# Kernel optimization log

Measured on AMD Instinct MI355X. Metric: run time of the kernel, lower is better.

## Reference

```python
import jax, jax.numpy as jnp
import numpy as np

N_NODES = 100000
N_EDGES = 1600000
DIM = 128
N_LAYERS = 3
BN_EPS = 1e-5


def setup_inputs() -> dict:
    key = jax.random.key(0)
    ks = jax.random.split(key, 8)
    x = jax.random.normal(ks[0], (N_NODES, DIM), dtype=jnp.float32)
    edge_index = jax.random.randint(ks[1], (2, N_EDGES), 0, N_NODES, dtype=jnp.int64)
    batch = jax.random.randint(ks[2], (N_NODES,), 0, 64, dtype=jnp.int64)
    # stacked per-layer params (input_dim == hidden_dim == 128)
    W = jax.random.normal(ks[3], (N_LAYERS, DIM, DIM), dtype=jnp.float32) / np.sqrt(DIM)
    b = jnp.zeros((N_LAYERS, DIM), dtype=jnp.float32)
    gamma = jax.random.normal(ks[4], (N_LAYERS, DIM), dtype=jnp.float32) * 0.1 + 1.0
    beta = jax.random.normal(ks[5], (N_LAYERS, DIM), dtype=jnp.float32) * 0.1
    running_mean = jax.random.normal(ks[6], (N_LAYERS, DIM), dtype=jnp.float32) * 0.1
    running_var = jax.random.uniform(ks[7], (N_LAYERS, DIM), dtype=jnp.float32, minval=0.5, maxval=1.5)
    return {"x": x, "edge_index": edge_index, "batch": batch, "W": W, "b": b,
            "gamma": gamma, "beta": beta,
            "running_mean": running_mean, "running_var": running_var}


def reference(x, edge_index, batch, W, b, gamma, beta, running_mean, running_var):
    # batch is unused by the original forward (kept for signature fidelity)
    n = x.shape[0]
    # GCNConv adds self-loops once per layer; precompute augmented edge list + norm
    loops = jnp.arange(n, dtype=edge_index.dtype)
    src = jnp.concatenate([edge_index[0], loops])
    dst = jnp.concatenate([edge_index[1], loops])
    deg = jax.ops.segment_sum(jnp.ones_like(dst, dtype=x.dtype), dst, num_segments=n)
    dinv = jax.lax.rsqrt(jnp.maximum(deg, 1e-12))
    norm = dinv[src] * dinv[dst]  # [E+N]

    h = x
    for l in range(N_LAYERS):
        # GCNConv: propagate normalized messages of (h @ W), then add bias
        hw = h @ W[l]                                   # [N, D]
        msg = hw[src] * norm[:, None]                   # gather  [E+N, D]
        h = jax.ops.segment_sum(msg, dst, num_segments=n) + b[l]
        # BatchNorm1d (eval mode: running stats) + ReLU; dropout is identity in eval
        h = gamma[l] * (h - running_mean[l]) * jax.lax.rsqrt(running_var[l] + BN_EPS) + beta[l]
        h = jax.nn.relu(h)
    return h
```

## Files before the change

kernel.cpp:

```cpp
#include <hip/hip_runtime.h>

#define N_NODES 100000
#define N_EDGES 1600000
#define DIM 128
#define BN_EPS 1e-5f
#define BM 64
#define BSHIFT 9
#define BN 512
#define NB 196
#define CAP_S 9216
#define CAP_C 10048
#define CHUNK 4096

typedef _Float16 f16;
typedef _Float16 f16x4 __attribute__((ext_vector_type(4)));
typedef _Float16 f16x8 __attribute__((ext_vector_type(8)));
typedef float f32x4 __attribute__((ext_vector_type(4)));


__global__ void k_bzero(int* __restrict__ bcnt) {
  int t = threadIdx.x;
  if (t < NB) bcnt[t] = 0;
}

__global__ __launch_bounds__(256) void k_binA(const int* __restrict__ src,
                                              const int* __restrict__ dst,
                                              int* __restrict__ bcnt,
                                              int2* __restrict__ stage) {
  __shared__ int hist[NB];
  __shared__ int lofs[NB];
  __shared__ int lbase[NB];
  __shared__ int lcur[NB];
  __shared__ int scanbuf[256];
  __shared__ int2 buf[CHUNK];
  int t = threadIdx.x;
  for (int i = t; i < NB; i += 256) { hist[i] = 0; lcur[i] = 0; }
  __syncthreads();
  int e0 = blockIdx.x * CHUNK;
  int en = min(CHUNK, N_EDGES - e0);
  for (int i = t; i < en; i += 256) {
    unsigned d = (unsigned)dst[e0 + i];
    unsigned s = (unsigned)src[e0 + i];
    if (d < N_NODES && s < N_NODES) atomicAdd(&hist[d >> BSHIFT], 1);
  }
  __syncthreads();
  scanbuf[t] = (t < NB) ? hist[t] : 0;
  __syncthreads();
  for (int off = 1; off < 256; off <<= 1) {
    int x = (t >= off) ? scanbuf[t - off] : 0;
    __syncthreads();
    scanbuf[t] += x;
    __syncthreads();
  }
  if (t < NB) {
    lofs[t] = scanbuf[t] - hist[t];
    lbase[t] = atomicAdd(&bcnt[t], hist[t]);
  }
  __syncthreads();
  for (int i = t; i < en; i += 256) {
    int d = dst[e0 + i], s = src[e0 + i];
    if ((unsigned)d < N_NODES && (unsigned)s < N_NODES) {
      int b = d >> BSHIFT;
      int r = atomicAdd(&lcur[b], 1);
      buf[lofs[b] + r] = make_int2(d, s);
    }
  }
  __syncthreads();
  int tot = lofs[NB - 1] + hist[NB - 1];
  for (int i = t; i < tot; i += 256) {
    int2 p = buf[i];
    int b = p.x >> BSHIFT;
    int goff = lbase[b] + (i - lofs[b]);
    if (goff < CAP_S) stage[(size_t)b * CAP_S + goff] = p;
  }
}

__global__ __launch_bounds__(512) void k_binB(const int2* __restrict__ stage,
                                              const int* __restrict__ bcnt,
                                              int* __restrict__ rowpack,
                                              int* __restrict__ col) {
  __shared__ int cnt[BN];
  __shared__ int offs[BN];
  __shared__ int lcur[BN];
  __shared__ int sb[BN];
  __shared__ int mp_s;
  __shared__ int colbuf[CAP_C];
  int b = blockIdx.x, t = threadIdx.x;
  int base = b << BSHIFT;
  int nn = min(BN, N_NODES - base);
  int m = min(bcnt[b], CAP_S);
  const int2* seg = stage + (size_t)b * CAP_S;
  cnt[t] = 0; lcur[t] = 0;
  __syncthreads();
  for (int i = t; i < m; i += 512) atomicAdd(&cnt[seg[i].x - base], 1);
  __syncthreads();
  int pcnt = (cnt[t] + 3) & ~3;
  sb[t] = pcnt;
  __syncthreads();
  for (int off = 1; off < 512; off <<= 1) {
    int x = (t >= off) ? sb[t - off] : 0;
    __syncthreads();
    sb[t] += x;
    __syncthreads();
  }
  offs[t] = sb[t] - pcnt;
  if (t == 511) mp_s = sb[511];
  __syncthreads();
  for (int i = t; i < m; i += 512) {
    int2 p = seg[i];
    int dl = p.x - base;
    int r = atomicAdd(&lcur[dl], 1);
    int o = offs[dl] + r;
    if (o < CAP_C) colbuf[o] = p.y;
  }
  __syncthreads();
  {
    int o = offs[t], c = cnt[t], pc = (c + 3) & ~3;
    for (int k = c; k < pc; k++)
      if (o + k < CAP_C) colbuf[o + k] = N_NODES;
  }
  __syncthreads();
  if (t < nn) {
    int o = offs[t], c = cnt[t];
    if (o + ((c + 3) & ~3) > CAP_C) { o = 0; c = 0; }
    rowpack[base + t] = (o << 14) | c;
  }
  int mp = min(mp_s, CAP_C);
  for (int i = t; i < mp; i += 512) col[b * CAP_C + i] = colbuf[i];
}


__global__ void k_x16(const float* __restrict__ x, f16* __restrict__ h16) {
  int i = blockIdx.x * blockDim.x + threadIdx.x;
  if (i < N_NODES * DIM / 4) {
    float4 v = ((const float4*)x)[i];
    f16x4 o = {(f16)v.x, (f16)v.y, (f16)v.z, (f16)v.w};
    ((f16x4*)h16)[i] = o;
  }
}

__global__ void k_wprep(const float* __restrict__ W, f16* __restrict__ Wt,
                        f16* __restrict__ hws) {
  int t = blockIdx.x * blockDim.x + threadIdx.x;
  if (t < DIM * DIM) {
    int c = t >> 7, k = t & 127;
    Wt[t] = (f16)W[k * DIM + c];
  }
  if (blockIdx.x == 0 && threadIdx.x < 16) {
    f16x8 z = {};
    ((f16x8*)(hws + (size_t)N_NODES * DIM))[threadIdx.x] = z;
  }
}

__global__ void k_bnprep(const float* __restrict__ b, const float* __restrict__ gamma,
                         const float* __restrict__ beta, const float* __restrict__ mean,
                         const float* __restrict__ var, float* __restrict__ scsh) {
  int t = threadIdx.x;
  if (t < 384) {
    int l = t >> 7, c = t & 127, i = l * DIM + c;
    float sc = gamma[i] * rsqrtf(var[i] + BN_EPS);
    scsh[l * 256 + c] = sc;
    scsh[l * 256 + 128 + c] = sc * (b[i] - mean[i]) + beta[i];
  }
}


__global__ __launch_bounds__(256) void k_gemm16(const f16* __restrict__ H16,
                                                const f16* __restrict__ Wt16,
                                                const int* __restrict__ rowpack,
                                                f16* __restrict__ HWS16) {
  __shared__ f16x8 Hs[BM * 16];
  __shared__ f16x8 WtS[DIM * 16];
  int t = threadIdx.x;
  int row0 = blockIdx.x * BM;

  const f16x8* Hg = (const f16x8*)H16;
  #pragma unroll
  for (int i = 0; i < 4; i++) {
    int q = t + i * 256;
    int r = q >> 4, s = q & 15;
    int gr = row0 + r; if (gr >= N_NODES) gr = N_NODES - 1;
    Hs[r * 16 + (s ^ (r & 7))] = Hg[(size_t)gr * 16 + s];
  }
  const f16x8* Wg = (const f16x8*)Wt16;
  #pragma unroll
  for (int i = 0; i < 8; i++) {
    int q = t + i * 256;
    int c = q >> 4, s = q & 15;
    WtS[c * 16 + (s ^ (c & 7))] = Wg[(size_t)c * 16 + s];
  }
  __syncthreads();

  int wid = t >> 6, l = t & 63;
  int wrow = wid * 16;
  int lr = l & 15, lg = l >> 4;

  int r = wrow + lr, rx = r & 7, rbase = r * 16;
  f16x8 afr[4];
  #pragma unroll
  for (int kk = 0; kk < 4; kk++) afr[kk] = Hs[rbase + ((kk * 4 + lg) ^ rx)];

  f32x4 acc[8] = {};
  #pragma unroll
  for (int ct = 0; ct < 8; ct++) {
    int c = ct * 16 + lr, cx = c & 7, cbase = c * 16;
    #pragma unroll
    for (int kk = 0; kk < 4; kk++) {
      f16x8 bfr = WtS[cbase + ((kk * 4 + lg) ^ cx)];
      acc[ct] = __builtin_amdgcn_mfma_f32_16x16x32_f16(afr[kk], bfr, acc[ct], 0, 0, 0);
    }
  }

  int orow = row0 + wrow + lg * 4;
  #pragma unroll
  for (int i = 0; i < 4; i++) {
    int gr = orow + i;
    if (gr < N_NODES) {
      float dv = rsqrtf((float)(rowpack[gr] & 0x3FFF) + 1.0f);
      #pragma unroll
      for (int ct = 0; ct < 8; ct++)
        HWS16[(size_t)gr * DIM + ct * 16 + lr] = (f16)(acc[ct][i] * dv);
    }
  }
}


__global__ __launch_bounds__(256) void k_gather8(const f16* __restrict__ HWS,
                                                 const int* __restrict__ rowpack,
                                                 const int* __restrict__ col,
                                                 const float* __restrict__ scsh,
                                                 float* __restrict__ outF,
                                                 f16* __restrict__ outH,
                                                 int last) {
  int tid = blockIdx.x * 256 + threadIdx.x;
  int wid = tid >> 4;
  int cs = tid & 15;
  if (wid >= N_NODES) return;
  int rp = rowpack[wid];
  int deg = rp & 0x3FFF;
  int off = rp >> 14;
  int pdeg = (deg + 3) & ~3;
  int beg = (wid >> BSHIFT) * CAP_C + off;
  const f16x8* h8 = (const f16x8*)HWS;

  f16x8 a0 = h8[(size_t)wid * 16 + cs];
  f16x8 a1 = {}, a2 = {}, a3 = {};
  int j = 0;
  for (; j + 8 <= pdeg; j += 8) {
    int4 c0 = *(const int4*)(col + beg + j);
    int4 c1 = *(const int4*)(col + beg + j + 4);
    f16x8 v0 = h8[(size_t)c0.x * 16 + cs];
    f16x8 v1 = h8[(size_t)c0.y * 16 + cs];
    f16x8 v2 = h8[(size_t)c0.z * 16 + cs];
    f16x8 v3 = h8[(size_t)c0.w * 16 + cs];
    f16x8 v4 = h8[(size_t)c1.x * 16 + cs];
    f16x8 v5 = h8[(size_t)c1.y * 16 + cs];
    f16x8 v6 = h8[(size_t)c1.z * 16 + cs];
    f16x8 v7 = h8[(size_t)c1.w * 16 + cs];
    a0 += v0; a1 += v1; a2 += v2; a3 += v3;
    a0 += v4; a1 += v5; a2 += v6; a3 += v7;
  }
  if (j < pdeg) {
    int4 c0 = *(const int4*)(col + beg + j);
    f16x8 v0 = h8[(size_t)c0.x * 16 + cs];
    f16x8 v1 = h8[(size_t)c0.y * 16 + cs];
    f16x8 v2 = h8[(size_t)c0.z * 16 + cs];
    f16x8 v3 = h8[(size_t)c0.w * 16 + cs];
    a0 += v0; a1 += v1; a2 += v2; a3 += v3;
  }
  a0 += a1; a2 += a3; a0 += a2;

  float di = rsqrtf((float)(deg + 1));
  int c4 = cs * 2;
  const f32x4* scv = (const f32x4*)scsh;
  const f32x4* shv = (const f32x4*)(scsh + 128);
  float o[8];
  #pragma unroll
  for (int half = 0; half < 2; half++) {
    f32x4 sc = scv[c4 + half], sh = shv[c4 + half];
    #pragma unroll
    for (int i = 0; i < 4; i++) {
      float v = (float)a0[half * 4 + i] * di;
      o[half * 4 + i] = fmaxf(fmaf(v, sc[i], sh[i]), 0.f);
    }
  }
  if (last) {
    f32x4* of = (f32x4*)outF;
    f32x4 lo = {o[0], o[1], o[2], o[3]}, hi = {o[4], o[5], o[6], o[7]};
    of[(size_t)wid * 32 + c4] = lo;
    of[(size_t)wid * 32 + c4 + 1] = hi;
  } else {
    f16x8 oh = {(f16)o[0], (f16)o[1], (f16)o[2], (f16)o[3],
                (f16)o[4], (f16)o[5], (f16)o[6], (f16)o[7]};
    ((f16x8*)outH)[(size_t)wid * 16 + cs] = oh;
  }
}


extern "C" void kernel_launch(void* const* d_in, const int* in_sizes, int n_in,
                              void* d_out, int out_size, void* d_ws, size_t ws_size,
                              hipStream_t stream) {
  const float* x = (const float*)d_in[0];
  const int* ei = (const int*)d_in[1];
  const int* srcv = ei;
  const int* dstv = ei + N_EDGES;
  const float* W     = (const float*)d_in[3];
  const float* b     = (const float*)d_in[4];
  const float* gamma = (const float*)d_in[5];
  const float* beta  = (const float*)d_in[6];
  const float* rmean = (const float*)d_in[7];
  const float* rvar  = (const float*)d_in[8];
  float* out = (float*)d_out;

  const size_t off_rowpack = 0;
  const size_t off_col     = 400128;
  const size_t off_scsh    = 400128 + 7877632;
  const size_t off_wt      = off_scsh + 3072;
  const size_t off_h16     = off_wt + 32768;
  const size_t off_hws     = off_h16 + 25600000;
  const size_t need = off_hws + (size_t)(N_NODES + 1) * DIM * sizeof(f16);
  if (ws_size < need) return;

  char* ws = (char*)d_ws;
  int*   rowpack = (int*)(ws + off_rowpack);
  int*   col     = (int*)(ws + off_col);
  float* scsh    = (float*)(ws + off_scsh);
  f16*   wt16    = (f16*)(ws + off_wt);
  f16*   h16     = (f16*)(ws + off_h16);
  int2*  stage   = (int2*)(ws + off_h16);
  f16*   hws16   = (f16*)(ws + off_hws);
  int*   bcnt    = (int*)(ws + off_hws);

  k_bzero<<<1, 256, 0, stream>>>(bcnt);
  k_binA<<<(N_EDGES + CHUNK - 1) / CHUNK, 256, 0, stream>>>(srcv, dstv, bcnt, stage);
  k_binB<<<NB, 512, 0, stream>>>(stage, bcnt, rowpack, col);
  k_x16<<<12500, 256, 0, stream>>>(x, h16);
  k_bnprep<<<1, 384, 0, stream>>>(b, gamma, beta, rmean, rvar, scsh);

  for (int l = 0; l < 3; l++) {
    k_wprep<<<64, 256, 0, stream>>>(W + l * DIM * DIM, wt16, hws16);
    k_gemm16<<<(N_NODES + BM - 1) / BM, 256, 0, stream>>>(h16, wt16, rowpack, hws16);
    k_gather8<<<6250, 256, 0, stream>>>(hws16, rowpack, col, scsh + l * 256,
                                        out, h16, (l == 2) ? 1 : 0);
  }
}
```

Before: 283.5 us.

## Split node features into eight column slices so the gather runs slice-local

```diff
diff --git a/kernel.cpp b/kernel.cpp
--- a/kernel.cpp
+++ b/kernel.cpp
@@ -11,11 +11,14 @@
 #define CAP_S 9216
 #define CAP_C 10048
 #define CHUNK 4096
+#define NSL 8
 
 typedef _Float16 f16;
 typedef _Float16 f16x4 __attribute__((ext_vector_type(4)));
 typedef _Float16 f16x8 __attribute__((ext_vector_type(8)));
 typedef float f32x4 __attribute__((ext_vector_type(4)));
+
+union h44 { f16x4 h[2]; f16x8 v; };
 
 
 __global__ void k_bzero(int* __restrict__ bcnt) {
@@ -130,12 +133,34 @@
 }
 
 
-__global__ void k_x16(const float* __restrict__ x, f16* __restrict__ h16) {
-  int i = blockIdx.x * blockDim.x + threadIdx.x;
-  if (i < N_NODES * DIM / 4) {
-    float4 v = ((const float4*)x)[i];
+__global__ __launch_bounds__(256) void k_xslice(const float* __restrict__ x,
+                                                f16* __restrict__ h16) {
+  __shared__ f16x4 lds[128 * 32];
+  int t = threadIdx.x;
+  int node0 = blockIdx.x * 128;
+  const float4* xf4 = (const float4*)x;
+  #pragma unroll
+  for (int i = 0; i < 16; i++) {
+    int q = t + i * 256;
+    int row = q >> 5, u = q & 31;
+    int gr = node0 + row; if (gr >= N_NODES) gr = N_NODES - 1;
+    float4 v = xf4[(size_t)gr * 32 + u];
     f16x4 o = {(f16)v.x, (f16)v.y, (f16)v.z, (f16)v.w};
-    ((f16x4*)h16)[i] = o;
+    lds[row * 32 + (u ^ ((row & 7) << 2))] = o;
+  }
+  __syncthreads();
+  f16x8* hg = (f16x8*)h16;
+  #pragma unroll
+  for (int i = 0; i < 8; i++) {
+    int q = t + i * 256;
+    int sl = q >> 8, rem = q & 255;
+    int row = rem >> 1, half = rem & 1;
+    int gr = node0 + row;
+    if (gr < N_NODES) {
+      int u0 = (sl * 4 + half * 2) ^ ((row & 7) << 2);
+      h44 c; c.h[0] = lds[row * 32 + u0]; c.h[1] = lds[row * 32 + u0 + 1];
+      hg[(size_t)(sl * N_NODES + gr) * 2 + half] = c.v;
+    }
   }
 }
 
@@ -147,8 +172,9 @@
     Wt[t] = (f16)W[k * DIM + c];
   }
   if (blockIdx.x == 0 && threadIdx.x < 16) {
+    int s = threadIdx.x >> 1, half = threadIdx.x & 1;
     f16x8 z = {};
-    ((f16x8*)(hws + (size_t)N_NODES * DIM))[threadIdx.x] = z;
+    ((f16x8*)hws)[(size_t)(s * (N_NODES + 1) + N_NODES) * 2 + half] = z;
   }
 }
 
@@ -178,9 +204,11 @@
   #pragma unroll
   for (int i = 0; i < 4; i++) {
     int q = t + i * 256;
-    int r = q >> 4, s = q & 15;
+    int sl = q >> 7, rem = q & 127;
+    int r = rem >> 1, half = rem & 1;
     int gr = row0 + r; if (gr >= N_NODES) gr = N_NODES - 1;
-    Hs[r * 16 + (s ^ (r & 7))] = Hg[(size_t)gr * 16 + s];
+    int s16 = sl * 2 + half;
+    Hs[r * 16 + (s16 ^ (r & 7))] = Hg[(size_t)(sl * N_NODES + gr) * 2 + half];
   }
   const f16x8* Wg = (const f16x8*)Wt16;
   #pragma unroll
@@ -219,22 +247,23 @@
       float dv = rsqrtf((float)(rowpack[gr] & 0x3FFF) + 1.0f);
       #pragma unroll
       for (int ct = 0; ct < 8; ct++)
-        HWS16[(size_t)gr * DIM + ct * 16 + lr] = (f16)(acc[ct][i] * dv);
-    }
-  }
-}
-
-
-__global__ __launch_bounds__(256) void k_gather8(const f16* __restrict__ HWS,
-                                                 const int* __restrict__ rowpack,
-                                                 const int* __restrict__ col,
-                                                 const float* __restrict__ scsh,
-                                                 float* __restrict__ outF,
-                                                 f16* __restrict__ outH,
-                                                 int last) {
-  int tid = blockIdx.x * 256 + threadIdx.x;
-  int wid = tid >> 4;
-  int cs = tid & 15;
+        HWS16[((size_t)ct * (N_NODES + 1) + gr) * 16 + lr] = (f16)(acc[ct][i] * dv);
+    }
+  }
+}
+
+
+__global__ __launch_bounds__(256) void k_gslice(const f16* __restrict__ HWS,
+                                                const int* __restrict__ rowpack,
+                                                const int* __restrict__ col,
+                                                const float* __restrict__ scsh,
+                                                float* __restrict__ outF,
+                                                f16* __restrict__ outH,
+                                                int last) {
+  int s = blockIdx.x & 7;
+  int t = threadIdx.x;
+  int wid = (blockIdx.x >> 3) * 128 + (t >> 1);
+  int half = t & 1;
   if (wid >= N_NODES) return;
   int rp = rowpack[wid];
   int deg = rp & 0x3FFF;
@@ -242,46 +271,47 @@
   int pdeg = (deg + 3) & ~3;
   int beg = (wid >> BSHIFT) * CAP_C + off;
   const f16x8* h8 = (const f16x8*)HWS;
-
-  f16x8 a0 = h8[(size_t)wid * 16 + cs];
+  size_t sbase = (size_t)s * (N_NODES + 1);
+
+  f16x8 a0 = h8[(sbase + wid) * 2 + half];
   f16x8 a1 = {}, a2 = {}, a3 = {};
   int j = 0;
   for (; j + 8 <= pdeg; j += 8) {
     int4 c0 = *(const int4*)(col + beg + j);
     int4 c1 = *(const int4*)(col + beg + j + 4);
-    f16x8 v0 = h8[(size_t)c0.x * 16 + cs];
-    f16x8 v1 = h8[(size_t)c0.y * 16 + cs];
-    f16x8 v2 = h8[(size_t)c0.z * 16 + cs];
-    f16x8 v3 = h8[(size_t)c0.w * 16 + cs];
-    f16x8 v4 = h8[(size_t)c1.x * 16 + cs];
-    f16x8 v5 = h8[(size_t)c1.y * 16 + cs];
-    f16x8 v6 = h8[(size_t)c1.z * 16 + cs];
-    f16x8 v7 = h8[(size_t)c1.w * 16 + cs];
+    f16x8 v0 = h8[(sbase + c0.x) * 2 + half];
+    f16x8 v1 = h8[(sbase + c0.y) * 2 + half];
+    f16x8 v2 = h8[(sbase + c0.z) * 2 + half];
+    f16x8 v3 = h8[(sbase + c0.w) * 2 + half];
+    f16x8 v4 = h8[(sbase + c1.x) * 2 + half];
+    f16x8 v5 = h8[(sbase + c1.y) * 2 + half];
+    f16x8 v6 = h8[(sbase + c1.z) * 2 + half];
+    f16x8 v7 = h8[(sbase + c1.w) * 2 + half];
     a0 += v0; a1 += v1; a2 += v2; a3 += v3;
     a0 += v4; a1 += v5; a2 += v6; a3 += v7;
   }
   if (j < pdeg) {
     int4 c0 = *(const int4*)(col + beg + j);
-    f16x8 v0 = h8[(size_t)c0.x * 16 + cs];
-    f16x8 v1 = h8[(size_t)c0.y * 16 + cs];
-    f16x8 v2 = h8[(size_t)c0.z * 16 + cs];
-    f16x8 v3 = h8[(size_t)c0.w * 16 + cs];
+    f16x8 v0 = h8[(sbase + c0.x) * 2 + half];
+    f16x8 v1 = h8[(sbase + c0.y) * 2 + half];
+    f16x8 v2 = h8[(sbase + c0.z) * 2 + half];
+    f16x8 v3 = h8[(sbase + c0.w) * 2 + half];
     a0 += v0; a1 += v1; a2 += v2; a3 += v3;
   }
   a0 += a1; a2 += a3; a0 += a2;
 
   float di = rsqrtf((float)(deg + 1));
-  int c4 = cs * 2;
+  int c4 = s * 4 + half * 2;
   const f32x4* scv = (const f32x4*)scsh;
   const f32x4* shv = (const f32x4*)(scsh + 128);
   float o[8];
   #pragma unroll
-  for (int half = 0; half < 2; half++) {
-    f32x4 sc = scv[c4 + half], sh = shv[c4 + half];
+  for (int hh = 0; hh < 2; hh++) {
+    f32x4 sc = scv[c4 + hh], sh = shv[c4 + hh];
     #pragma unroll
     for (int i = 0; i < 4; i++) {
-      float v = (float)a0[half * 4 + i] * di;
-      o[half * 4 + i] = fmaxf(fmaf(v, sc[i], sh[i]), 0.f);
+      float v = (float)a0[hh * 4 + i] * di;
+      o[hh * 4 + i] = fmaxf(fmaf(v, sc[i], sh[i]), 0.f);
     }
   }
   if (last) {
@@ -292,7 +322,7 @@
   } else {
     f16x8 oh = {(f16)o[0], (f16)o[1], (f16)o[2], (f16)o[3],
                 (f16)o[4], (f16)o[5], (f16)o[6], (f16)o[7]};
-    ((f16x8*)outH)[(size_t)wid * 16 + cs] = oh;
+    ((f16x8*)outH)[(size_t)(s * N_NODES + wid) * 2 + half] = oh;
   }
 }
 
@@ -318,7 +348,7 @@
   const size_t off_wt      = off_scsh + 3072;
   const size_t off_h16     = off_wt + 32768;
   const size_t off_hws     = off_h16 + 25600000;
-  const size_t need = off_hws + (size_t)(N_NODES + 1) * DIM * sizeof(f16);
+  const size_t need = off_hws + (size_t)NSL * (N_NODES + 1) * 32;
   if (ws_size < need) return;
 
   char* ws = (char*)d_ws;
@@ -334,13 +364,13 @@
   k_bzero<<<1, 256, 0, stream>>>(bcnt);
   k_binA<<<(N_EDGES + CHUNK - 1) / CHUNK, 256, 0, stream>>>(srcv, dstv, bcnt, stage);
   k_binB<<<NB, 512, 0, stream>>>(stage, bcnt, rowpack, col);
-  k_x16<<<12500, 256, 0, stream>>>(x, h16);
+  k_xslice<<<782, 256, 0, stream>>>(x, h16);
   k_bnprep<<<1, 384, 0, stream>>>(b, gamma, beta, rmean, rvar, scsh);
 
   for (int l = 0; l < 3; l++) {
     k_wprep<<<64, 256, 0, stream>>>(W + l * DIM * DIM, wt16, hws16);
     k_gemm16<<<(N_NODES + BM - 1) / BM, 256, 0, stream>>>(h16, wt16, rowpack, hws16);
-    k_gather8<<<6250, 256, 0, stream>>>(hws16, rowpack, col, scsh + l * 256,
-                                        out, h16, (l == 2) ? 1 : 0);
-  }
-}
+    k_gslice<<<8 * 782, 256, 0, stream>>>(hws16, rowpack, col, scsh + l * 256,
+                                          out, h16, (l == 2) ? 1 : 0);
+  }
+}
```

Measured after the change: 344.5 us. 1.22x slower.

## Fuse gather+BN+ReLU with next layer GEMM and merge prep kernels

Applied to the files above, without the earlier changes.

```diff
diff --git a/kernel.cpp b/kernel.cpp
--- a/kernel.cpp
+++ b/kernel.cpp
@@ -4,7 +4,6 @@
 #define N_EDGES 1600000
 #define DIM 128
 #define BN_EPS 1e-5f
-#define BM 64
 #define BSHIFT 9
 #define BN 512
 #define NB 196
@@ -17,11 +16,6 @@
 typedef _Float16 f16x8 __attribute__((ext_vector_type(8)));
 typedef float f32x4 __attribute__((ext_vector_type(4)));
 
-
-__global__ void k_bzero(int* __restrict__ bcnt) {
-  int t = threadIdx.x;
-  if (t < NB) bcnt[t] = 0;
-}
 
 __global__ __launch_bounds__(256) void k_binA(const int* __restrict__ src,
                                               const int* __restrict__ dst,
@@ -130,59 +124,60 @@
 }
 
 
-__global__ void k_x16(const float* __restrict__ x, f16* __restrict__ h16) {
-  int i = blockIdx.x * blockDim.x + threadIdx.x;
-  if (i < N_NODES * DIM / 4) {
-    float4 v = ((const float4*)x)[i];
-    f16x4 o = {(f16)v.x, (f16)v.y, (f16)v.z, (f16)v.w};
-    ((f16x4*)h16)[i] = o;
-  }
-}
-
-__global__ void k_wprep(const float* __restrict__ W, f16* __restrict__ Wt,
-                        f16* __restrict__ hws) {
-  int t = blockIdx.x * blockDim.x + threadIdx.x;
-  if (t < DIM * DIM) {
-    int c = t >> 7, k = t & 127;
-    Wt[t] = (f16)W[k * DIM + c];
-  }
-  if (blockIdx.x == 0 && threadIdx.x < 16) {
-    f16x8 z = {};
-    ((f16x8*)(hws + (size_t)N_NODES * DIM))[threadIdx.x] = z;
-  }
-}
-
-__global__ void k_bnprep(const float* __restrict__ b, const float* __restrict__ gamma,
-                         const float* __restrict__ beta, const float* __restrict__ mean,
-                         const float* __restrict__ var, float* __restrict__ scsh) {
-  int t = threadIdx.x;
-  if (t < 384) {
-    int l = t >> 7, c = t & 127, i = l * DIM + c;
+__global__ __launch_bounds__(256) void k_prep(const float* __restrict__ W,
+                                              const float* __restrict__ bb,
+                                              const float* __restrict__ gamma,
+                                              const float* __restrict__ beta,
+                                              const float* __restrict__ mean,
+                                              const float* __restrict__ var,
+                                              f16* __restrict__ wt,
+                                              float* __restrict__ scsh,
+                                              f16* __restrict__ hwsA,
+                                              f16* __restrict__ hwsB,
+                                              int* __restrict__ bcnt) {
+  int tg = blockIdx.x * 256 + threadIdx.x;
+  if (tg < 3 * DIM * DIM) {
+    int l = tg / (DIM * DIM), r = tg % (DIM * DIM);
+    int c = r >> 7, k = r & 127;
+    wt[tg] = (f16)W[l * DIM * DIM + k * DIM + c];
+  }
+  if (tg < 384) {
+    int l = tg >> 7, c = tg & 127, i = l * DIM + c;
     float sc = gamma[i] * rsqrtf(var[i] + BN_EPS);
     scsh[l * 256 + c] = sc;
-    scsh[l * 256 + 128 + c] = sc * (b[i] - mean[i]) + beta[i];
-  }
-}
-
-
-__global__ __launch_bounds__(256) void k_gemm16(const f16* __restrict__ H16,
-                                                const f16* __restrict__ Wt16,
-                                                const int* __restrict__ rowpack,
-                                                f16* __restrict__ HWS16) {
-  __shared__ f16x8 Hs[BM * 16];
+    scsh[l * 256 + 128 + c] = sc * (bb[i] - mean[i]) + beta[i];
+  }
+  if (tg >= 49152 && tg < 49152 + 32) {
+    int i = tg - 49152;
+    f16x8 z = {};
+    f16x8* p = (i < 16) ? (f16x8*)hwsA : (f16x8*)hwsB;
+    p[(size_t)N_NODES * 16 + (i & 15)] = z;
+  }
+  if (tg >= 49184 && tg < 49184 + NB) bcnt[tg - 49184] = 0;
+}
+
+
+__global__ __launch_bounds__(256) void k_gemm0(const float* __restrict__ x,
+                                               const f16* __restrict__ wt,
+                                               const int* __restrict__ rowpack,
+                                               f16* __restrict__ HWS) {
+  __shared__ f16x8 Hs[64 * 16];
   __shared__ f16x8 WtS[DIM * 16];
   int t = threadIdx.x;
-  int row0 = blockIdx.x * BM;
-
-  const f16x8* Hg = (const f16x8*)H16;
+  int row0 = blockIdx.x * 64;
+  const float4* xf = (const float4*)x;
   #pragma unroll
   for (int i = 0; i < 4; i++) {
     int q = t + i * 256;
     int r = q >> 4, s = q & 15;
     int gr = row0 + r; if (gr >= N_NODES) gr = N_NODES - 1;
-    Hs[r * 16 + (s ^ (r & 7))] = Hg[(size_t)gr * 16 + s];
-  }
-  const f16x8* Wg = (const f16x8*)Wt16;
+    float4 u0 = xf[(size_t)gr * 32 + s * 2];
+    float4 u1 = xf[(size_t)gr * 32 + s * 2 + 1];
+    f16x8 o = {(f16)u0.x, (f16)u0.y, (f16)u0.z, (f16)u0.w,
+               (f16)u1.x, (f16)u1.y, (f16)u1.z, (f16)u1.w};
+    Hs[r * 16 + (s ^ (r & 7))] = o;
+  }
+  const f16x8* Wg = (const f16x8*)wt;
   #pragma unroll
   for (int i = 0; i < 8; i++) {
     int q = t + i * 256;
@@ -194,7 +189,6 @@
   int wid = t >> 6, l = t & 63;
   int wrow = wid * 16;
   int lr = l & 15, lg = l >> 4;
-
   int r = wrow + lr, rx = r & 7, rbase = r * 16;
   f16x8 afr[4];
   #pragma unroll
@@ -210,7 +204,6 @@
       acc[ct] = __builtin_amdgcn_mfma_f32_16x16x32_f16(afr[kk], bfr, acc[ct], 0, 0, 0);
     }
   }
-
   int orow = row0 + wrow + lg * 4;
   #pragma unroll
   for (int i = 0; i < 4; i++) {
@@ -219,19 +212,103 @@
       float dv = rsqrtf((float)(rowpack[gr] & 0x3FFF) + 1.0f);
       #pragma unroll
       for (int ct = 0; ct < 8; ct++)
-        HWS16[(size_t)gr * DIM + ct * 16 + lr] = (f16)(acc[ct][i] * dv);
-    }
-  }
-}
-
-
-__global__ __launch_bounds__(256) void k_gather8(const f16* __restrict__ HWS,
-                                                 const int* __restrict__ rowpack,
-                                                 const int* __restrict__ col,
-                                                 const float* __restrict__ scsh,
-                                                 float* __restrict__ outF,
-                                                 f16* __restrict__ outH,
-                                                 int last) {
+        HWS[(size_t)gr * DIM + ct * 16 + lr] = (f16)(acc[ct][i] * dv);
+    }
+  }
+}
+
+
+__global__ __launch_bounds__(256) void k_fused(const f16* __restrict__ hwsIn,
+                                               const f16* __restrict__ wt,
+                                               const int* __restrict__ rowpack,
+                                               const int* __restrict__ col,
+                                               const float* __restrict__ scsh,
+                                               f16* __restrict__ hwsOut) {
+  __shared__ f16x8 Hs[64 * 16];
+  int t = threadIdx.x;
+  int row = t >> 2;
+  int qd = t & 3;
+  int n = blockIdx.x * 64 + row;
+  int rp = (n < N_NODES) ? rowpack[n] : 0;
+  int deg = rp & 0x3FFF, off = rp >> 14;
+  int pdeg = (deg + 3) & ~3;
+  int beg = (n >> BSHIFT) * CAP_C + off;
+  int selfrow = (n < N_NODES) ? n : N_NODES;
+  const f16x8* h8 = (const f16x8*)hwsIn;
+
+  size_t sbs = (size_t)selfrow * 16 + qd * 4;
+  f16x8 aA0 = h8[sbs], aA1 = h8[sbs + 1], aA2 = h8[sbs + 2], aA3 = h8[sbs + 3];
+  f16x8 aB0 = {}, aB1 = {}, aB2 = {}, aB3 = {};
+  for (int j = 0; j + 2 <= pdeg; j += 2) {
+    int2 c2 = *(const int2*)(col + beg + j);
+    size_t b0 = (size_t)c2.x * 16 + qd * 4;
+    size_t b1 = (size_t)c2.y * 16 + qd * 4;
+    f16x8 v0 = h8[b0], v1 = h8[b0 + 1], v2 = h8[b0 + 2], v3 = h8[b0 + 3];
+    f16x8 w0 = h8[b1], w1 = h8[b1 + 1], w2 = h8[b1 + 2], w3 = h8[b1 + 3];
+    aA0 += v0; aA1 += v1; aA2 += v2; aA3 += v3;
+    aB0 += w0; aB1 += w1; aB2 += w2; aB3 += w3;
+  }
+  aA0 += aB0; aA1 += aB1; aA2 += aB2; aA3 += aB3;
+
+  float di = rsqrtf((float)(deg + 1));
+  const f32x4* scv = (const f32x4*)scsh;
+  const f32x4* shv = (const f32x4*)(scsh + 128);
+  f16x8 accs[4] = {aA0, aA1, aA2, aA3};
+  #pragma unroll
+  for (int k = 0; k < 4; k++) {
+    int s = qd * 4 + k;
+    f32x4 sc0 = scv[s * 2], sh0 = shv[s * 2];
+    f32x4 sc1 = scv[s * 2 + 1], sh1 = shv[s * 2 + 1];
+    f16x8 o;
+    #pragma unroll
+    for (int i = 0; i < 4; i++)
+      o[i] = (f16)fmaxf(fmaf((float)accs[k][i] * di, sc0[i], sh0[i]), 0.f);
+    #pragma unroll
+    for (int i = 0; i < 4; i++)
+      o[4 + i] = (f16)fmaxf(fmaf((float)accs[k][4 + i] * di, sc1[i], sh1[i]), 0.f);
+    Hs[row * 16 + (s ^ (row & 7))] = o;
+  }
+  __syncthreads();
+
+  int wid = t >> 6, l = t & 63;
+  int wrow = wid * 16;
+  int lr = l & 15, lg = l >> 4;
+  int r = wrow + lr, rx = r & 7, rbase = r * 16;
+  f16x8 afr[4];
+  #pragma unroll
+  for (int kk = 0; kk < 4; kk++) afr[kk] = Hs[rbase + ((kk * 4 + lg) ^ rx)];
+
+  const f16x8* Wg = (const f16x8*)wt;
+  f32x4 acc[8] = {};
+  #pragma unroll
+  for (int ct = 0; ct < 8; ct++) {
+    int c = ct * 16 + lr;
+    #pragma unroll
+    for (int kk = 0; kk < 4; kk++) {
+      f16x8 bfr = Wg[(size_t)c * 16 + kk * 4 + lg];
+      acc[ct] = __builtin_amdgcn_mfma_f32_16x16x32_f16(afr[kk], bfr, acc[ct], 0, 0, 0);
+    }
+  }
+  int row0 = blockIdx.x * 64;
+  int orow = row0 + wrow + lg * 4;
+  #pragma unroll
+  for (int i = 0; i < 4; i++) {
+    int gr = orow + i;
+    if (gr < N_NODES) {
+      float dv = rsqrtf((float)(rowpack[gr] & 0x3FFF) + 1.0f);
+      #pragma unroll
+      for (int ct = 0; ct < 8; ct++)
+        hwsOut[(size_t)gr * DIM + ct * 16 + lr] = (f16)(acc[ct][i] * dv);
+    }
+  }
+}
+
+
+__global__ __launch_bounds__(256) void k_gatherout(const f16* __restrict__ HWS,
+                                                   const int* __restrict__ rowpack,
+                                                   const int* __restrict__ col,
+                                                   const float* __restrict__ scsh,
+                                                   float* __restrict__ outF) {
   int tid = blockIdx.x * 256 + threadIdx.x;
   int wid = tid >> 4;
   int cs = tid & 15;
@@ -284,16 +361,10 @@
       o[half * 4 + i] = fmaxf(fmaf(v, sc[i], sh[i]), 0.f);
     }
   }
-  if (last) {
-    f32x4* of = (f32x4*)outF;
-    f32x4 lo = {o[0], o[1], o[2], o[3]}, hi = {o[4], o[5], o[6], o[7]};
-    of[(size_t)wid * 32 + c4] = lo;
-    of[(size_t)wid * 32 + c4 + 1] = hi;
-  } else {
-    f16x8 oh = {(f16)o[0], (f16)o[1], (f16)o[2], (f16)o[3],
-                (f16)o[4], (f16)o[5], (f16)o[6], (f16)o[7]};
-    ((f16x8*)outH)[(size_t)wid * 16 + cs] = oh;
-  }
+  f32x4* of = (f32x4*)outF;
+  f32x4 lo = {o[0], o[1], o[2], o[3]}, hi = {o[4], o[5], o[6], o[7]};
+  of[(size_t)wid * 32 + c4] = lo;
+  of[(size_t)wid * 32 + c4 + 1] = hi;
 }
 
 
@@ -316,31 +387,30 @@
   const size_t off_col     = 400128;
   const size_t off_scsh    = 400128 + 7877632;
   const size_t off_wt      = off_scsh + 3072;
-  const size_t off_h16     = off_wt + 32768;
-  const size_t off_hws     = off_h16 + 25600000;
-  const size_t need = off_hws + (size_t)(N_NODES + 1) * DIM * sizeof(f16);
+  const size_t off_hwsB    = off_wt + 98304;
+  const size_t off_hwsA    = off_hwsB + 25600256;
+  const size_t need = off_hwsA + 25600256;
   if (ws_size < need) return;
 
   char* ws = (char*)d_ws;
   int*   rowpack = (int*)(ws + off_rowpack);
   int*   col     = (int*)(ws + off_col);
   float* scsh    = (float*)(ws + off_scsh);
-  f16*   wt16    = (f16*)(ws + off_wt);
-  f16*   h16     = (f16*)(ws + off_h16);
-  int2*  stage   = (int2*)(ws + off_h16);
-  f16*   hws16   = (f16*)(ws + off_hws);
-  int*   bcnt    = (int*)(ws + off_hws);
-
-  k_bzero<<<1, 256, 0, stream>>>(bcnt);
+  f16*   wt      = (f16*)(ws + off_wt);
+  f16*   hwsB    = (f16*)(ws + off_hwsB);
+  f16*   hwsA    = (f16*)(ws + off_hwsA);
+  int2*  stage   = (int2*)(ws + off_hwsB);
+  int*   bcnt    = (int*)(ws + off_hwsA);
+
+  k_prep<<<193, 256, 0, stream>>>(W, b, gamma, beta, rmean, rvar,
+                                  wt, scsh, hwsA, hwsB, bcnt);
   k_binA<<<(N_EDGES + CHUNK - 1) / CHUNK, 256, 0, stream>>>(srcv, dstv, bcnt, stage);
   k_binB<<<NB, 512, 0, stream>>>(stage, bcnt, rowpack, col);
-  k_x16<<<12500, 256, 0, stream>>>(x, h16);
-  k_bnprep<<<1, 384, 0, stream>>>(b, gamma, beta, rmean, rvar, scsh);
-
-  for (int l = 0; l < 3; l++) {
-    k_wprep<<<64, 256, 0, stream>>>(W + l * DIM * DIM, wt16, hws16);
-    k_gemm16<<<(N_NODES + BM - 1) / BM, 256, 0, stream>>>(h16, wt16, rowpack, hws16);
-    k_gather8<<<6250, 256, 0, stream>>>(hws16, rowpack, col, scsh + l * 256,
-                                        out, h16, (l == 2) ? 1 : 0);
-  }
-}
+
+  k_gemm0<<<1563, 256, 0, stream>>>(x, wt, rowpack, hwsA);
+  k_fused<<<1563, 256, 0, stream>>>(hwsA, wt + DIM * DIM, rowpack, col,
+                                    scsh, hwsB);
+  k_fused<<<1563, 256, 0, stream>>>(hwsB, wt + 2 * DIM * DIM, rowpack, col,
+                                    scsh + 256, hwsA);
+  k_gatherout<<<6250, 256, 0, stream>>>(hwsA, rowpack, col, scsh + 512, out);
+}
```

Result: slower. 321.1 us (+13.3%).
